# Kernel optimization log

Hardware: AMD Instinct MI355X
Metric: run time of the kernel (lower is better)

## Reference

```python
import jax, jax.numpy as jnp
import numpy as np

N_EMBD = 768
N_HEAD = 12
EPS = 1e-5


def _layernorm(x, g, b):
    mu = jnp.mean(x, axis=-1, keepdims=True)
    var = jnp.var(x, axis=-1, keepdims=True)
    return (x - mu) * jax.lax.rsqrt(var + EPS) * g + b


def setup_inputs() -> dict:
    key = jax.random.key(0)
    ks = jax.random.split(key, 12)
    C = N_EMBD
    s = 0.02
    return {
        "x": jax.random.normal(ks[0], (1, 4096, C), dtype=jnp.float32),
        "ln1_g": jnp.ones((C,), jnp.float32),
        "ln1_b": jnp.zeros((C,), jnp.float32),
        "w_attn": jax.random.normal(ks[1], (C, 3 * C), jnp.float32) * s,
        "b_attn": jnp.zeros((3 * C,), jnp.float32),
        "w_ao": jax.random.normal(ks[2], (C, C), jnp.float32) * s,
        "b_ao": jnp.zeros((C,), jnp.float32),
        "ln2_g": jnp.ones((C,), jnp.float32),
        "ln2_b": jnp.zeros((C,), jnp.float32),
        "w_fc": jax.random.normal(ks[3], (C, 4 * C), jnp.float32) * s,
        "b_fc": jnp.zeros((4 * C,), jnp.float32),
        "w_proj": jax.random.normal(ks[4], (4 * C, C), jnp.float32) * s,
        "b_proj": jnp.zeros((C,), jnp.float32),
    }


def reference(x, ln1_g, ln1_b, w_attn, b_attn, w_ao, b_ao,
              ln2_g, ln2_b, w_fc, b_fc, w_proj, b_proj):
    B, T, C = x.shape
    H = N_HEAD
    D = C // H

    # ---- attention sub-block ----
    h = _layernorm(x, ln1_g, ln1_b)
    qkv = h @ w_attn + b_attn                      # [B,T,3C]
    q, k, v = jnp.split(qkv, 3, axis=-1)
    q = q.reshape(B, T, H, D).transpose(0, 2, 1, 3)  # [B,H,T,D]
    k = k.reshape(B, T, H, D).transpose(0, 2, 1, 3)
    v = v.reshape(B, T, H, D).transpose(0, 2, 1, 3)
    att = jnp.einsum('bhqd,bhkd->bhqk', q, k) * (1.0 / jnp.sqrt(jnp.float32(D)))
    att = jax.nn.softmax(att, axis=-1)             # no causal mask in source
    y = jnp.einsum('bhqk,bhkd->bhqd', att, v)      # [B,H,T,D]
    y = y.transpose(0, 2, 1, 3).reshape(B, T, C)
    x = x + y @ w_ao + b_ao

    # ---- MLP sub-block ----
    h = _layernorm(x, ln2_g, ln2_b)
    h = jax.nn.gelu(h @ w_fc + b_fc, approximate=False)  # torch F.gelu = exact
    x = x + h @ w_proj + b_proj
    return x
```

## Files before the change

kernel.cpp:

```cpp
#include <hip/hip_runtime.h>
#include <hip/hip_bf16.h>
#include <cstdint>
#include <cstddef>

typedef __hip_bfloat16 bf16;
typedef __attribute__((ext_vector_type(8))) short short8;
typedef __attribute__((ext_vector_type(4))) float f32x4;
typedef __attribute__((ext_vector_type(16))) float f32x16;

#define C_EMBD 768
#define C3     2304
#define T_SEQ  4096
#define NHEAD  12
#define KVSPLIT 2

__device__ __forceinline__ void load16(const void* g, void* lds) {
  __builtin_amdgcn_global_load_lds(
      (const __attribute__((address_space(1))) uint32_t*)g,
      (__attribute__((address_space(3))) uint32_t*)lds, 16, 0, 0);
}

__device__ __forceinline__ short f2bf_bits(float x) {
  union { bf16 h; short s; } u; u.h = __float2bfloat16(x); return u.s;
}

__device__ __forceinline__ float bfbits2f(short s) {
  union { uint32_t u; float f; } u; u.u = ((uint32_t)(unsigned short)s) << 16; return u.f;
}

__device__ __forceinline__ float max3f(float a, float b, float c) {
  float d;
  asm("v_max3_f32 %0, %1, %2, %3" : "=v"(d) : "v"(a), "v"(b), "v"(c));
  return d;
}

#if __has_builtin(__builtin_amdgcn_exp2f)
#define QK_SCALE (0.125f * 1.44269504088896340736f)
__device__ __forceinline__ float expx(float x) { return __builtin_amdgcn_exp2f(x); }
#else
#define QK_SCALE 0.125f
__device__ __forceinline__ float expx(float x) { return __expf(x); }
#endif

__global__ __launch_bounds__(256) void ln2_fused_kernel(
    const float* __restrict__ pa0, const float* __restrict__ pa1,
    const float* __restrict__ x, const float* __restrict__ b_ao,
    const float* __restrict__ g, const float* __restrict__ b,
    bf16* __restrict__ out, float* __restrict__ x1) {
  const int row = blockIdx.x;
  const int tid = threadIdx.x;
  const int lane = tid & 63, wave = tid >> 6;
  float v[3];
  #pragma unroll
  for (int i = 0; i < 3; ++i) {
    const int c = tid + i * 256;
    const size_t idx = (size_t)row * C_EMBD + c;
    v[i] = pa0[idx] + pa1[idx] + x[idx] + b_ao[c];
    x1[idx] = v[i];
  }
  float s = v[0] + v[1] + v[2];
  #pragma unroll
  for (int o = 1; o < 64; o <<= 1) s += __shfl_xor(s, o, 64);
  __shared__ float red[4];
  if (lane == 0) red[wave] = s;
  __syncthreads();
  const float mu = (red[0] + red[1] + red[2] + red[3]) * (1.0f / C_EMBD);
  float d0 = v[0] - mu, d1 = v[1] - mu, d2 = v[2] - mu;
  float q = d0 * d0 + d1 * d1 + d2 * d2;
  #pragma unroll
  for (int o = 1; o < 64; o <<= 1) q += __shfl_xor(q, o, 64);
  __syncthreads();
  if (lane == 0) red[wave] = q;
  __syncthreads();
  const float var = (red[0] + red[1] + red[2] + red[3]) * (1.0f / C_EMBD);
  const float rs = rsqrtf(var + 1e-5f);
  #pragma unroll
  for (int i = 0; i < 3; ++i) {
    int c = tid + i * 256;
    out[(size_t)row * C_EMBD + c] = __float2bfloat16((v[i] - mu) * rs * g[c] + b[c]);
  }
}

__global__ __launch_bounds__(256) void transpose4_ln_kernel(
    const float* __restrict__ wA, bf16* __restrict__ oA,
    const float* __restrict__ wB, bf16* __restrict__ oB,
    const float* __restrict__ wC, bf16* __restrict__ oC,
    const float* __restrict__ wD, bf16* __restrict__ oD,
    const float* __restrict__ x, const float* __restrict__ lg,
    const float* __restrict__ lb, bf16* __restrict__ oh) {
  __shared__ float tile[32][33];
  __shared__ float red[4];
  int b = blockIdx.x;
  if (b >= 6912) {
    const int row = b - 6912;
    const int tid = threadIdx.y * 32 + threadIdx.x;
    const int lane = tid & 63, wave = tid >> 6;
    const float* xr = x + (size_t)row * C_EMBD;
    float v[3];
    #pragma unroll
    for (int i = 0; i < 3; ++i) v[i] = xr[tid + i * 256];
    float s = v[0] + v[1] + v[2];
    #pragma unroll
    for (int o = 1; o < 64; o <<= 1) s += __shfl_xor(s, o, 64);
    if (lane == 0) red[wave] = s;
    __syncthreads();
    const float mu = (red[0] + red[1] + red[2] + red[3]) * (1.0f / C_EMBD);
    float d0 = v[0] - mu, d1 = v[1] - mu, d2 = v[2] - mu;
    float q = d0 * d0 + d1 * d1 + d2 * d2;
    #pragma unroll
    for (int o = 1; o < 64; o <<= 1) q += __shfl_xor(q, o, 64);
    __syncthreads();
    if (lane == 0) red[wave] = q;
    __syncthreads();
    const float var = (red[0] + red[1] + red[2] + red[3]) * (1.0f / C_EMBD);
    const float rs = rsqrtf(var + 1e-5f);
    #pragma unroll
    for (int i = 0; i < 3; ++i) {
      int c = tid + i * 256;
      oh[(size_t)row * C_EMBD + c] = __float2bfloat16((v[i] - mu) * rs * lg[c] + lb[c]);
    }
    return;
  }
  const float* in; bf16* out; int R, C;
  if (b < 1728)      { in = wA; out = oA; R = 768;  C = 2304; }
  else if (b < 2304) { b -= 1728; in = wB; out = oB; R = 768;  C = 768;  }
  else if (b < 4608) { b -= 2304; in = wC; out = oC; R = 768;  C = 3072; }
  else               { b -= 4608; in = wD; out = oD; R = 3072; C = 768;  }
  const int ntx = C / 32;
  const int bx = (b % ntx) * 32;
  const int by = (b / ntx) * 32;
  const int tx = threadIdx.x, ty = threadIdx.y;
  #pragma unroll
  for (int i = 0; i < 32; i += 8)
    tile[ty + i][tx] = in[(size_t)(by + ty + i) * C + bx + tx];
  __syncthreads();
  #pragma unroll
  for (int i = 0; i < 32; i += 8)
    out[(size_t)(bx + ty + i) * R + by + tx] = __float2bfloat16(tile[tx][ty + i]);
}

template <int EPI>
__global__ __launch_bounds__(256, 3) void gemm_bt(
    const bf16* __restrict__ A, const bf16* __restrict__ BT,
    const float* __restrict__ bias, const float* __restrict__ res,
    void* __restrict__ outp, float* __restrict__ outp2, int M, int N, int Ks, int Kst) {
  __shared__ __align__(16) short sA[2][128 * 32];
  __shared__ __align__(16) short sB[2][128 * 32];
  const int tid = threadIdx.x;
  const int wave = tid >> 6, lane = tid & 63;
  const int qr = lane >> 4, qm = lane & 15;
  const int wr = wave >> 1, wc = wave & 1;
  const int gx = gridDim.x;
  int flat = blockIdx.y * gx + blockIdx.x;
  const int cpx = (gx * gridDim.y) >> 3;
  flat = (flat & 7) * cpx + (flat >> 3);
  const int tM = (flat / gx) * 128, tN = (flat % gx) * 128;
  const int z = (EPI == 4) ? blockIdx.z : 0;

  f32x4 acc[4][4] = {};

  const int srow = tid >> 2;
  const int scol = (tid & 3) * 8;
  const bf16* gA = A + (size_t)z * Ks + (size_t)(tM + srow) * Kst + scol;
  const bf16* gB = BT + (size_t)z * Ks + (size_t)(tN + srow) * Kst + scol;
  const int woff = wave * 1024;
  const size_t rowskip = (size_t)64 * Kst;

  const int nk = Ks >> 5;
  {
    char* la = (char*)sA[0] + woff;
    char* lb = (char*)sB[0] + woff;
    load16(gA, la);
    load16(gA + rowskip, la + 4096);
    load16(gB, lb);
    load16(gB + rowskip, lb + 4096);
    gA += 32; gB += 32;
  }
  __syncthreads();

  int cur = 0;
  for (int k0 = 0; k0 < nk; ++k0) {
    if (k0 + 1 < nk) {
      char* la = (char*)sA[cur ^ 1] + woff;
      char* lb = (char*)sB[cur ^ 1] + woff;
      load16(gA, la);
      load16(gA + rowskip, la + 4096);
      load16(gB, lb);
      load16(gB + rowskip, lb + 4096);
      gA += 32; gB += 32;
    }
    const short* bufA = sA[cur];
    const short* bufB = sB[cur];
    short8 a[4], bb[4];
    #pragma unroll
    for (int i = 0; i < 4; ++i) {
      a[i]  = *(const short8*)&bufA[(wr * 64 + i * 16 + qm) * 32 + qr * 8];
      bb[i] = *(const short8*)&bufB[(wc * 64 + i * 16 + qm) * 32 + qr * 8];
    }
    #pragma unroll
    for (int mi = 0; mi < 4; ++mi)
      #pragma unroll
      for (int ni = 0; ni < 4; ++ni)
        acc[mi][ni] = __builtin_amdgcn_mfma_f32_16x16x32_bf16(a[mi], bb[ni], acc[mi][ni], 0, 0, 0);
    __syncthreads();
    cur ^= 1;
  }

  bf16* outh = (bf16*)outp;
  float* po = (EPI == 4) ? ((z == 0) ? (float*)outp : outp2) : nullptr;
  #pragma unroll
  for (int mi = 0; mi < 4; ++mi) {
    #pragma unroll
    for (int ni = 0; ni < 4; ++ni) {
      const int col = tN + wc * 64 + ni * 16 + qm;
      const float bv = (EPI == 4) ? 0.f : bias[col];
      #pragma unroll
      for (int r = 0; r < 4; ++r) {
        const int row = tM + wr * 64 + mi * 16 + qr * 4 + r;
        const size_t idx = (size_t)row * N + col;
        float v = acc[mi][ni][r] + bv;
        if constexpr (EPI == 4) {
          po[idx] = v;
        } else if constexpr (EPI == 2) {
          v = 0.5f * v * (1.0f + erff(v * 0.70710678118654752f));
          outh[idx] = __float2bfloat16(v);
        } else {
          outh[idx] = __float2bfloat16(v);
        }
      }
    }
  }
  (void)res;
}

__global__ __launch_bounds__(256) void splitk_combine(const float* p0,
    const float* __restrict__ p1, const float* __restrict__ res,
    const float* __restrict__ bias, float* out) {
  const int row = blockIdx.x;
  const int tid = threadIdx.x;
  #pragma unroll
  for (int i = 0; i < 3; ++i) {
    const int c = tid + i * 256;
    const size_t idx = (size_t)row * C_EMBD + c;
    out[idx] = p0[idx] + p1[idx] + res[idx] + bias[c];
  }
}

__global__ __launch_bounds__(256, 2) void attn_kernel(const bf16* __restrict__ qkv,
                                                      float* __restrict__ pacc,
                                                      float* __restrict__ pml) {
  __shared__ __align__(16) char sKb[2 * 8192];
  __shared__ __align__(16) char sVb[2 * 8192];
  __shared__ float sRed[4 * 32];

  const int tid = threadIdx.x;
  const int wave = tid >> 6, lane = tid & 63;
  const int qi = lane & 31;
  const int hi = lane >> 5;
  const int hi16 = hi * 16;
  const int head = blockIdx.y;
  const int z = blockIdx.z;
  const int qw = blockIdx.x * 128 + wave * 32;

  short8 qf[4];
  {
    const bf16* qrow = qkv + (size_t)(qw + qi) * C3 + head * 64;
    #pragma unroll
    for (int kd = 0; kd < 4; ++kd) {
      short8 v = *(const short8*)(qrow + kd * 16 + hi * 8);
      #pragma unroll
      for (int i = 0; i < 8; ++i) v[i] = f2bf_bits(bfbits2f(v[i]) * QK_SCALE);
      qf[kd] = v;
    }
  }

  f32x16 acc0 = {}, acc1 = {};
  float m = -3.0e38f, l = 0.f;
  short8 pfrag[4];

  const int nt = (T_SEQ / 64) / KVSPLIT;
  const size_t tilestep = (size_t)64 * C3;
  const size_t zoff = (size_t)z * nt * tilestep;
  const int ksrow = tid >> 3;
  const int kswz = ((tid & 7) ^ (ksrow & 7)) * 8;
  const bf16* gk_base = qkv + zoff + (size_t)ksrow * C3 + C_EMBD + head * 64 + kswz;
  const int vp = tid & 31;
  const int vd0 = (tid >> 5) * 8;
  const bf16* gv_base = qkv + zoff + (size_t)(2 * vp) * C3 + 2 * C_EMBD + head * 64 + vd0;

  const int krow0 = qi * 128;
  const int krow_swz = (qi & 7) << 4;
  const int d1 = 32 + qi;
  const int vs0 = ((qi & 7) ^ ((qi >> 3) & 7)) << 4;
  const int vs1 = ((d1 & 7) ^ ((d1 >> 3) & 7)) << 4;

  short8 v0 = *(const short8*)gv_base;
  short8 v1 = *(const short8*)(gv_base + C3);
  load16(gk_base, sKb + wave * 1024);
  load16(gk_base + (size_t)32 * C3, sKb + wave * 1024 + 4096);

  for (int t = 0; t < nt; ++t) {
    const int cur = t & 1;
    char* bK = sKb + cur * 8192;
    char* bV = sVb + cur * 8192;

    __syncthreads();

    #pragma unroll
    for (int j = 0; j < 8; ++j) {
      const int d = vd0 + j;
      const int vs = ((d & 7) ^ ((d >> 3) & 7)) << 4;
      const uint32_t packed = (uint32_t)(unsigned short)v0[j] |
                              ((uint32_t)(unsigned short)v1[j] << 16);
      *(uint32_t*)(bV + d * 128 + ((vp * 4) ^ vs)) = packed;
    }

    if (t + 1 < nt) {
      const bf16* gv = gv_base + (size_t)(t + 1) * tilestep;
      v0 = *(const short8*)gv;
      v1 = *(const short8*)(gv + C3);
      const bf16* gk = gk_base + (size_t)(t + 1) * tilestep;
      char* bKn = sKb + (cur ^ 1) * 8192;
      load16(gk, bKn + wave * 1024);
      load16(gk + (size_t)32 * C3, bKn + wave * 1024 + 4096);
    }

    f32x16 s0 = {}, s1 = {};
    __builtin_amdgcn_s_setprio(1);
    #pragma unroll
    for (int kd = 0; kd < 4; ++kd) {
      const int off = (kd * 32 + hi16) ^ krow_swz;
      short8 ka0 = *(const short8*)(bK + krow0 + off);
      short8 ka1 = *(const short8*)(bK + 4096 + krow0 + off);
      s0 = __builtin_amdgcn_mfma_f32_32x32x16_bf16(ka0, qf[kd], s0, 0, 0, 0);
      s1 = __builtin_amdgcn_mfma_f32_32x32x16_bf16(ka1, qf[kd], s1, 0, 0, 0);
    }

    if (t > 0) {
      char* bVp = sVb + (cur ^ 1) * 8192;
      #pragma unroll
      for (int kk = 0; kk < 4; ++kk) {
        const int voff = (kk * 32 + hi16);
        short8 vb0 = *(const short8*)(bVp + qi * 128 + (voff ^ vs0));
        short8 vb1 = *(const short8*)(bVp + d1 * 128 + (voff ^ vs1));
        acc0 = __builtin_amdgcn_mfma_f32_32x32x16_bf16(pfrag[kk], vb0, acc0, 0, 0, 0);
        acc1 = __builtin_amdgcn_mfma_f32_32x32x16_bf16(pfrag[kk], vb1, acc1, 0, 0, 0);
      }
    }
    __builtin_amdgcn_s_setprio(0);

    float t8[8];
    #pragma unroll
    for (int i = 0; i < 8; ++i) t8[i] = max3f(s0[i], s0[i + 8], s1[i]);
    float t4[4];
    #pragma unroll
    for (int i = 0; i < 4; ++i) t4[i] = max3f(t8[2 * i], t8[2 * i + 1], s1[8 + i]);
    float t2[2];
    #pragma unroll
    for (int i = 0; i < 2; ++i) t2[i] = max3f(t4[2 * i], t4[2 * i + 1], s1[12 + i]);
    const float t1 = max3f(t2[0], t2[1], s1[14]);
    const float tmx = fmaxf(t1, s1[15]);
    float pmax;
    {
      float a0 = tmx, a1 = tmx;
      asm("v_permlane32_swap_b32 %0, %1" : "+v"(a0), "+v"(a1));
      pmax = fmaxf(a0, a1);
    }

    if (__any(pmax - m > 8.0f)) {
      const float mn = fmaxf(m, pmax);
      const float sc = expx(m - mn);
      l *= sc;
      if (lane < 32) sRed[wave * 32 + qi] = sc;
      #pragma unroll
      for (int r = 0; r < 16; ++r) {
        const float sv = sRed[wave * 32 + ((r & 3) + 8 * (r >> 2) + hi * 4)];
        acc0[r] *= sv; acc1[r] *= sv;
      }
      m = mn;
    }

    float red[16];
    #pragma unroll
    for (int r = 0; r < 16; ++r) { s0[r] = expx(s0[r] - m); s1[r] = expx(s1[r] - m); }
    #pragma unroll
    for (int r = 0; r < 16; ++r) red[r] = s0[r] + s1[r];
    #pragma unroll
    for (int w = 8; w >= 1; w >>= 1)
      #pragma unroll
      for (int r = 0; r < w; ++r) red[r] += red[r + w];
    {
      float a0 = red[0], a1 = red[0];
      asm("v_permlane32_swap_b32 %0, %1" : "+v"(a0), "+v"(a1));
      l += a0 + a1;
    }

    #pragma unroll
    for (int b = 0; b < 2; ++b) {
      const f32x16 sb = b ? s1 : s0;
      uint32_t pk[8];
      #pragma unroll
      for (int g = 0; g < 4; ++g) {
        asm("v_cvt_pk_bf16_f32 %0, %1, %2" : "=v"(pk[2 * g])     : "v"(sb[4 * g + 0]), "v"(sb[4 * g + 1]));
        asm("v_cvt_pk_bf16_f32 %0, %1, %2" : "=v"(pk[2 * g + 1]) : "v"(sb[4 * g + 2]), "v"(sb[4 * g + 3]));
      }
      #pragma unroll
      for (int kbl = 0; kbl < 2; ++kbl) {
        uint32_t w0 = pk[4 * kbl + 0], w2 = pk[4 * kbl + 2];
        asm("v_permlane32_swap_b32 %0, %1" : "+v"(w0), "+v"(w2));
        uint32_t w1 = pk[4 * kbl + 1], w3 = pk[4 * kbl + 3];
        asm("v_permlane32_swap_b32 %0, %1" : "+v"(w1), "+v"(w3));
        union { uint32_t u[4]; short8 v; } pu;
        pu.u[0] = w0; pu.u[1] = w1; pu.u[2] = w2; pu.u[3] = w3;
        pfrag[b * 2 + kbl] = pu.v;
      }
    }
  }

  __syncthreads();
  {
    char* bVl = sVb + ((nt - 1) & 1) * 8192;
    __builtin_amdgcn_s_setprio(1);
    #pragma unroll
    for (int kk = 0; kk < 4; ++kk) {
      const int voff = (kk * 32 + hi16);
      short8 vb0 = *(const short8*)(bVl + qi * 128 + (voff ^ vs0));
      short8 vb1 = *(const short8*)(bVl + d1 * 128 + (voff ^ vs1));
      acc0 = __builtin_amdgcn_mfma_f32_32x32x16_bf16(pfrag[kk], vb0, acc0, 0, 0, 0);
      acc1 = __builtin_amdgcn_mfma_f32_32x32x16_bf16(pfrag[kk], vb1, acc1, 0, 0, 0);
    }
    __builtin_amdgcn_s_setprio(0);
  }

  float* pa = pacc + ((size_t)z * T_SEQ + qw) * C_EMBD + head * 64;
  #pragma unroll
  for (int r = 0; r < 16; ++r) {
    const int q = (r & 3) + 8 * (r >> 2) + hi * 4;
    pa[(size_t)q * C_EMBD + qi]      = acc0[r];
    pa[(size_t)q * C_EMBD + 32 + qi] = acc1[r];
  }
  if (lane < 32) {
    float2* mlp = (float2*)pml;
    mlp[((size_t)z * NHEAD + head) * T_SEQ + qw + qi] = make_float2(m, l);
  }
}

__global__ __launch_bounds__(256) void attn_combine(const float* __restrict__ pacc,
    const float* __restrict__ pml, bf16* __restrict__ out) {
  const int q = blockIdx.x;
  const int tid = threadIdx.x;
  const float2* mlp = (const float2*)pml;
  #pragma unroll
  for (int i = 0; i < 3; ++i) {
    const int c = tid + i * 256;
    const int h = c >> 6;
    const float2 ml0 = mlp[(size_t)h * T_SEQ + q];
    const float2 ml1 = mlp[((size_t)NHEAD + h) * T_SEQ + q];
    const float M = fmaxf(ml0.x, ml1.x);
    const float w0 = expx(ml0.x - M), w1 = expx(ml1.x - M);
    const float inv = 1.0f / (ml0.y * w0 + ml1.y * w1);
    const float a0 = pacc[(size_t)q * C_EMBD + c];
    const float a1 = pacc[(size_t)T_SEQ * C_EMBD + (size_t)q * C_EMBD + c];
    out[(size_t)q * C_EMBD + c] = __float2bfloat16((a0 * w0 + a1 * w1) * inv);
  }
}

extern "C" void kernel_launch(void* const* d_in, const int* in_sizes, int n_in,
                              void* d_out, int out_size, void* d_ws, size_t ws_size,
                              hipStream_t stream) {
  const float* x      = (const float*)d_in[0];
  const float* ln1_g  = (const float*)d_in[1];
  const float* ln1_b  = (const float*)d_in[2];
  const float* w_attn = (const float*)d_in[3];
  const float* b_attn = (const float*)d_in[4];
  const float* w_ao   = (const float*)d_in[5];
  const float* b_ao   = (const float*)d_in[6];
  const float* ln2_g  = (const float*)d_in[7];
  const float* ln2_b  = (const float*)d_in[8];
  const float* w_fc   = (const float*)d_in[9];
  const float* b_fc   = (const float*)d_in[10];
  const float* w_proj = (const float*)d_in[11];
  const float* b_proj = (const float*)d_in[12];

  char* ws = (char*)d_ws;
  size_t off = 0;
  auto alloc = [&](size_t nbytes) {
    char* p = ws + off;
    off += (nbytes + 255) & ~(size_t)255;
    return p;
  };
  bf16* wT_attn = (bf16*)alloc((size_t)C3 * C_EMBD * 2);
  bf16* wT_ao   = (bf16*)alloc((size_t)C_EMBD * C_EMBD * 2);
  bf16* wT_fc   = (bf16*)alloc((size_t)4 * C_EMBD * C_EMBD * 2);
  bf16* wT_proj = (bf16*)alloc((size_t)C_EMBD * 4 * C_EMBD * 2);
  bf16* h       = (bf16*)alloc((size_t)T_SEQ * C_EMBD * 2);
  bf16* qkv     = (bf16*)alloc((size_t)T_SEQ * C3 * 2);
  bf16* y       = (bf16*)alloc((size_t)T_SEQ * C_EMBD * 2);
  float* x1     = (float*)alloc((size_t)T_SEQ * C_EMBD * 4);
  bf16* hf      = (bf16*)alloc((size_t)T_SEQ * 4 * C_EMBD * 2);
  float* pml    = (float*)alloc((size_t)KVSPLIT * NHEAD * T_SEQ * 2 * 4);
  float* pacc   = (float*)hf;
  float* pa0    = (float*)hf;
  float* pa1    = (float*)hf + (size_t)T_SEQ * C_EMBD;
  float* pp0    = (float*)d_out;
  float* pp1    = (float*)qkv;
  (void)ws_size; (void)in_sizes; (void)n_in; (void)out_size;

  transpose4_ln_kernel<<<6912 + T_SEQ, dim3(32, 8), 0, stream>>>(
      w_attn, wT_attn, w_ao, wT_ao, w_fc, wT_fc, w_proj, wT_proj,
      x, ln1_g, ln1_b, h);

  gemm_bt<0><<<dim3(C3 / 128, T_SEQ / 128), 256, 0, stream>>>(h, wT_attn, b_attn, nullptr, qkv,
                                                              nullptr, T_SEQ, C3, C_EMBD, C_EMBD);
  attn_kernel<<<dim3(T_SEQ / 128, NHEAD, KVSPLIT), 256, 0, stream>>>(qkv, pacc, pml);
  attn_combine<<<T_SEQ, 256, 0, stream>>>(pacc, pml, y);
  gemm_bt<4><<<dim3(C_EMBD / 128, T_SEQ / 128, 2), 256, 0, stream>>>(y, wT_ao, nullptr, nullptr,
                                                                     pa0, pa1, T_SEQ, C_EMBD,
                                                                     C_EMBD / 2, C_EMBD);
  ln2_fused_kernel<<<T_SEQ, 256, 0, stream>>>(pa0, pa1, x, b_ao, ln2_g, ln2_b, h, x1);
  gemm_bt<2><<<dim3(4 * C_EMBD / 128, T_SEQ / 128), 256, 0, stream>>>(h, wT_fc, b_fc, nullptr, hf,
                                                                      nullptr, T_SEQ, 4 * C_EMBD,
                                                                      C_EMBD, C_EMBD);
  gemm_bt<4><<<dim3(C_EMBD / 128, T_SEQ / 128, 2), 256, 0, stream>>>(hf, wT_proj, nullptr, nullptr,
                                                                     pp0, pp1, T_SEQ, C_EMBD,
                                                                     2 * C_EMBD, 4 * C_EMBD);
  splitk_combine<<<T_SEQ, 256, 0, stream>>>(pp0, pp1, x1, b_proj, (float*)d_out);
}
```

Baseline: 220.6 us.

## Move three weight transposes into attention kernel as extra blocks

The transpose-and-convert of w_ao, w_fc and w_proj moves out of the first kernel and into the attention kernel as trailing blocks, using the K shared-memory buffer as the tile. Only the w_attn transpose stays ahead of the QKV GEMM, so the critical path before that GEMM gets shorter. The other transposes run beside attention and fill idle compute units in its tail. The attention grid is flattened to 1D with head and split indices computed from the block id. The trade-off is that the transpose blocks compete for memory bandwidth with attention, and the attention kernel's launch bounds and LDS footprint now also apply to them.

```diff
diff --git a/kernel.cpp b/kernel.cpp
--- a/kernel.cpp
+++ b/kernel.cpp
@@ -81,19 +81,16 @@
   }
 }
 
-__global__ __launch_bounds__(256) void transpose4_ln_kernel(
+__global__ __launch_bounds__(256) void transpose1_ln_kernel(
     const float* __restrict__ wA, bf16* __restrict__ oA,
-    const float* __restrict__ wB, bf16* __restrict__ oB,
-    const float* __restrict__ wC, bf16* __restrict__ oC,
-    const float* __restrict__ wD, bf16* __restrict__ oD,
     const float* __restrict__ x, const float* __restrict__ lg,
     const float* __restrict__ lb, bf16* __restrict__ oh) {
   __shared__ float tile[32][33];
   __shared__ float red[4];
   int b = blockIdx.x;
-  if (b >= 6912) {
-    const int row = b - 6912;
-    const int tid = threadIdx.y * 32 + threadIdx.x;
+  const int tid = threadIdx.x;
+  if (b >= 1728) {
+    const int row = b - 1728;
     const int lane = tid & 63, wave = tid >> 6;
     const float* xr = x + (size_t)row * C_EMBD;
     float v[3];
@@ -121,22 +118,17 @@
     }
     return;
   }
-  const float* in; bf16* out; int R, C;
-  if (b < 1728)      { in = wA; out = oA; R = 768;  C = 2304; }
-  else if (b < 2304) { b -= 1728; in = wB; out = oB; R = 768;  C = 768;  }
-  else if (b < 4608) { b -= 2304; in = wC; out = oC; R = 768;  C = 3072; }
-  else               { b -= 4608; in = wD; out = oD; R = 3072; C = 768;  }
-  const int ntx = C / 32;
+  const int ntx = C3 / 32;
   const int bx = (b % ntx) * 32;
   const int by = (b / ntx) * 32;
-  const int tx = threadIdx.x, ty = threadIdx.y;
+  const int tx = tid & 31, ty = tid >> 5;
   #pragma unroll
   for (int i = 0; i < 32; i += 8)
-    tile[ty + i][tx] = in[(size_t)(by + ty + i) * C + bx + tx];
+    tile[ty + i][tx] = wA[(size_t)(by + ty + i) * C3 + bx + tx];
   __syncthreads();
   #pragma unroll
   for (int i = 0; i < 32; i += 8)
-    out[(size_t)(bx + ty + i) * R + by + tx] = __float2bfloat16(tile[tx][ty + i]);
+    oA[(size_t)(bx + ty + i) * C_EMBD + by + tx] = __float2bfloat16(tile[tx][ty + i]);
 }
 
 template <int EPI>
@@ -246,21 +238,47 @@
   }
 }
 
-__global__ __launch_bounds__(256, 2) void attn_kernel(const bf16* __restrict__ qkv,
-                                                      float* __restrict__ pacc,
-                                                      float* __restrict__ pml) {
+__global__ __launch_bounds__(256, 2) void attn_tr_kernel(const bf16* __restrict__ qkv,
+                                                         float* __restrict__ pacc,
+                                                         float* __restrict__ pml,
+                                                         const float* __restrict__ wB, bf16* __restrict__ oB,
+                                                         const float* __restrict__ wC, bf16* __restrict__ oC,
+                                                         const float* __restrict__ wD, bf16* __restrict__ oD) {
   __shared__ __align__(16) char sKb[2 * 8192];
   __shared__ __align__(16) char sVb[2 * 8192];
   __shared__ float sRed[4 * 32];
 
   const int tid = threadIdx.x;
+  const int bid = blockIdx.x;
+
+  if (bid >= 768) {
+    int b = bid - 768;
+    const float* in; bf16* out; int R, C;
+    if (b < 576)       { in = wB; out = oB; R = 768;  C = 768;  }
+    else if (b < 2880) { b -= 576;  in = wC; out = oC; R = 768;  C = 3072; }
+    else               { b -= 2880; in = wD; out = oD; R = 3072; C = 768;  }
+    float (*tile)[33] = (float(*)[33])sKb;
+    const int ntx = C / 32;
+    const int bx = (b % ntx) * 32;
+    const int by = (b / ntx) * 32;
+    const int tx = tid & 31, ty = tid >> 5;
+    #pragma unroll
+    for (int i = 0; i < 32; i += 8)
+      tile[ty + i][tx] = in[(size_t)(by + ty + i) * C + bx + tx];
+    __syncthreads();
+    #pragma unroll
+    for (int i = 0; i < 32; i += 8)
+      out[(size_t)(bx + ty + i) * R + by + tx] = __float2bfloat16(tile[tx][ty + i]);
+    return;
+  }
+
   const int wave = tid >> 6, lane = tid & 63;
   const int qi = lane & 31;
   const int hi = lane >> 5;
   const int hi16 = hi * 16;
-  const int head = blockIdx.y;
-  const int z = blockIdx.z;
-  const int qw = blockIdx.x * 128 + wave * 32;
+  const int head = (bid >> 5) % NHEAD;
+  const int z = bid / (32 * NHEAD);
+  const int qw = (bid & 31) * 128 + wave * 32;
 
   short8 qf[4];
   {
@@ -506,13 +524,12 @@
   float* pp1    = (float*)qkv;
   (void)ws_size; (void)in_sizes; (void)n_in; (void)out_size;
 
-  transpose4_ln_kernel<<<6912 + T_SEQ, dim3(32, 8), 0, stream>>>(
-      w_attn, wT_attn, w_ao, wT_ao, w_fc, wT_fc, w_proj, wT_proj,
-      x, ln1_g, ln1_b, h);
+  transpose1_ln_kernel<<<1728 + T_SEQ, 256, 0, stream>>>(w_attn, wT_attn, x, ln1_g, ln1_b, h);
 
   gemm_bt<0><<<dim3(C3 / 128, T_SEQ / 128), 256, 0, stream>>>(h, wT_attn, b_attn, nullptr, qkv,
                                                               nullptr, T_SEQ, C3, C_EMBD, C_EMBD);
-  attn_kernel<<<dim3(T_SEQ / 128, NHEAD, KVSPLIT), 256, 0, stream>>>(qkv, pacc, pml);
+  attn_tr_kernel<<<768 + 5184, 256, 0, stream>>>(qkv, pacc, pml,
+                                                 w_ao, wT_ao, w_fc, wT_fc, w_proj, wT_proj);
   attn_combine<<<T_SEQ, 256, 0, stream>>>(pacc, pml, y);
   gemm_bt<4><<<dim3(C_EMBD / 128, T_SEQ / 128, 2), 256, 0, stream>>>(y, wT_ao, nullptr, nullptr,
                                                                      pa0, pa1, T_SEQ, C_EMBD,
```

After: 216.8 us. About the same (-1.7%).
